# Optimization experiments

Measured on AMD Instinct MI355X. Metric: run time of the kernel, lower is better.

Reference implementation:

```python
import jax, jax.numpy as jnp
import numpy as np

N = 1 << 20          # ray samples
POS_DIM = 32         # levels * feature_dim (hash_encoding is identity stub)
DENSITY_W = 64
COLOR_W = 64


def sh4_encoding(d):
    # Fourth-order (degree-4, 16-component) real spherical harmonics, vectorized.
    x, y, z = d[..., 0], d[..., 1], d[..., 2]
    xx, yy, zz = x * x, y * y, z * z
    c0 = jnp.full_like(x, 0.28209479177387814)
    comps = [
        c0,
        0.4886025119029199 * y,
        0.4886025119029199 * z,
        0.4886025119029199 * x,
        1.0925484305920792 * x * y,
        1.0925484305920792 * y * z,
        0.9461746957575601 * zz - 0.31539156525252,
        1.0925484305920792 * x * z,
        0.5462742152960396 * (xx - yy),
        0.5900435899266435 * y * (3 * xx - yy),
        2.890611442640554 * x * y * z,
        0.4570457994644658 * y * (5 * zz - 1),
        0.3731763325901154 * z * (5 * zz - 3),
        0.4570457994644658 * x * (5 * zz - 1),
        1.445305721320277 * z * (xx - yy),
        0.5900435899266435 * x * (xx - 3 * yy),
    ]
    return jnp.stack(comps, axis=-1)  # [..., 16]


def setup_inputs() -> dict:
    key = jax.random.key(0)
    ks = jax.random.split(key, 8)
    def dense_init(k, fan_in, fan_out):
        # flax default: lecun_normal kernel, zeros bias
        w = jax.random.normal(k, (fan_in, fan_out), dtype=jnp.float32) / np.sqrt(fan_in)
        b = jnp.zeros((fan_out,), dtype=jnp.float32)
        return w, b
    position = jax.random.normal(ks[0], (N, POS_DIM), dtype=jnp.float32)
    direction = jax.random.normal(ks[1], (N, 3), dtype=jnp.float32)
    W1, b1 = dense_init(ks[2], POS_DIM, DENSITY_W)
    W2, b2 = dense_init(ks[3], DENSITY_W, 16)
    W3, b3 = dense_init(ks[4], 16 + 16, COLOR_W)
    W4, b4 = dense_init(ks[5], COLOR_W, COLOR_W)
    W5, b5 = dense_init(ks[6], COLOR_W, 3)
    return {
        "position": position, "direction": direction,
        "W1": W1, "b1": b1, "W2": W2, "b2": b2,
        "W3": W3, "b3": b3, "W4": W4, "b4": b4,
        "W5": W5, "b5": b5,
    }


def reference(position, direction, W1, b1, W2, b2, W3, b3, W4, b4, W5, b5):
    # Density MLP
    h = jax.nn.relu(position @ W1 + b1)        # [N, 64]
    density = h @ W2 + b2                      # [N, 16]
    # Color MLP on concat(density_feat, SH(dir))
    enc_dir = sh4_encoding(direction)          # [N, 16]
    c = jnp.concatenate([density, enc_dir], axis=-1)  # [N, 32]
    c = jax.nn.relu(c @ W3 + b3)               # [N, 64]
    c = jax.nn.relu(c @ W4 + b4)               # [N, 64]
    c = c @ W5 + b5                            # [N, 3]
    color = jax.nn.sigmoid(c)                  # high_dynamic_range=False
    return (density, color)
```

## Files before the change

kernel.cpp:

```cpp
#include <hip/hip_runtime.h>
#include <hip/hip_bf16.h>

typedef __bf16 bf16_t;
typedef short  s4    __attribute__((ext_vector_type(4)));
typedef short  s8    __attribute__((ext_vector_type(8)));
typedef float  f32x4 __attribute__((ext_vector_type(4)));

#define TPW   16
#define WAVES 4
#define ROWS_PER_BLOCK (WAVES * TPW * 16)

__device__ __forceinline__ short bfs(float f) {
    return __builtin_bit_cast(short, (bf16_t)f);
}
__device__ __forceinline__ s4 pack4(f32x4 a) {
    s4 r; r[0]=bfs(a[0]); r[1]=bfs(a[1]); r[2]=bfs(a[2]); r[3]=bfs(a[3]); return r;
}
__device__ __forceinline__ s4 relu_pack4(f32x4 a) {
    s4 r;
    r[0]=bfs(fmaxf(a[0],0.f)); r[1]=bfs(fmaxf(a[1],0.f));
    r[2]=bfs(fmaxf(a[2],0.f)); r[3]=bfs(fmaxf(a[3],0.f));
    return r;
}
__device__ __forceinline__ s8 cat(s4 a, s4 b) {
    return __builtin_shufflevector(a, b, 0, 1, 2, 3, 4, 5, 6, 7);
}
#define MFMA32(a,b,c) __builtin_amdgcn_mfma_f32_16x16x32_bf16(a, b, c, 0, 0, 0)

__global__ __launch_bounds__(256) void nerf_fused(
    const float* __restrict__ pos, const float* __restrict__ dir,
    const float* __restrict__ W1, const float* __restrict__ b1,
    const float* __restrict__ W2, const float* __restrict__ b2,
    const float* __restrict__ W3, const float* __restrict__ b3,
    const float* __restrict__ W4, const float* __restrict__ b4,
    const float* __restrict__ W5, const float* __restrict__ b5,
    float* __restrict__ outD, float* __restrict__ outC)
{
    const int tid  = threadIdx.x;
    const int w    = tid >> 6;
    const int lane = tid & 63;
    const int q    = lane >> 4;
    const int n    = lane & 15;

    s8 wa1[4], wa2x[2], wa3[4], wa4x[4][2], wa5x[2];
    #pragma unroll
    for (int t = 0; t < 4; ++t)
        #pragma unroll
        for (int h = 0; h < 2; ++h)
            #pragma unroll
            for (int i = 0; i < 4; ++i)
                wa1[t][4*h+i] = bfs(W1[(16*h + 4*q + i) * 64 + 16*t + n]);
    #pragma unroll
    for (int j = 0; j < 2; ++j)
        #pragma unroll
        for (int h = 0; h < 2; ++h)
            #pragma unroll
            for (int i = 0; i < 4; ++i)
                wa2x[j][4*h+i] = bfs(W2[(16*(2*j+h) + 4*q + i) * 16 + n]);
    #pragma unroll
    for (int t = 0; t < 4; ++t)
        #pragma unroll
        for (int h = 0; h < 2; ++h)
            #pragma unroll
            for (int i = 0; i < 4; ++i)
                wa3[t][4*h+i] = bfs(W3[(16*h + 4*q + i) * 64 + 16*t + n]);
    #pragma unroll
    for (int t = 0; t < 4; ++t)
        #pragma unroll
        for (int j = 0; j < 2; ++j)
            #pragma unroll
            for (int h = 0; h < 2; ++h)
                #pragma unroll
                for (int i = 0; i < 4; ++i)
                    wa4x[t][j][4*h+i] = bfs(W4[(16*(2*j+h) + 4*q + i) * 64 + 16*t + n]);
    #pragma unroll
    for (int j = 0; j < 2; ++j)
        #pragma unroll
        for (int h = 0; h < 2; ++h)
            #pragma unroll
            for (int i = 0; i < 4; ++i)
                wa5x[j][4*h+i] = (n < 3) ? bfs(W5[(16*(2*j+h) + 4*q + i) * 3 + n])
                                         : (short)0;

    f32x4 bi1[4], bi3[4], bi4[4], bi2, bi5;
    #pragma unroll
    for (int t = 0; t < 4; ++t)
        #pragma unroll
        for (int r = 0; r < 4; ++r) {
            bi1[t][r] = b1[16*t + 4*q + r];
            bi3[t][r] = b3[16*t + 4*q + r];
            bi4[t][r] = b4[16*t + 4*q + r];
        }
    #pragma unroll
    for (int r = 0; r < 4; ++r) {
        bi2[r] = b2[4*q + r];
        bi5[r] = (q == 0 && r < 3) ? b5[r] : 0.f;
    }

    const int waveRow0 = blockIdx.x * ROWS_PER_BLOCK + w * (TPW * 16);

    const float* pp = pos  + (size_t)(waveRow0 + n) * 32 + 4*q;
    const float* dp = dir  + (size_t)(waveRow0 + n) * 3;
    float*       pD = outD + (size_t)(waveRow0 + n) * 16 + 4*q;
    float*       pC = outC + (size_t)(waveRow0 + n) * 3;

    f32x4 pa = *(const f32x4*)pp;
    f32x4 pb = *(const f32x4*)(pp + 16);
    float dx = dp[0];
    float dy = dp[1];
    float dz = dp[2];

    for (int t = 0; t < TPW; ++t) {
        const float* ppn = pp + ((t + 1 < TPW) ? 16 * 32 : 0);
        const float* dpn = dp + ((t + 1 < TPW) ? 16 * 3  : 0);
        f32x4 pa2 = *(const f32x4*)ppn;
        f32x4 pb2 = *(const f32x4*)(ppn + 16);
        float dx2 = dpn[0];
        float dy2 = dpn[1];
        float dz2 = dpn[2];

        s8 xb = cat(pack4(pa), pack4(pb));

        s4 hf[4];
        #pragma unroll
        for (int tt = 0; tt < 4; ++tt) {
            f32x4 h = MFMA32(wa1[tt], xb, bi1[tt]);
            hf[tt] = relu_pack4(h);
        }

        f32x4 d2 = MFMA32(wa2x[0], cat(hf[0], hf[1]), bi2);
        d2 = MFMA32(wa2x[1], cat(hf[2], hf[3]), d2);

        *(f32x4*)pD = d2;

        f32x4 shv;
        {
            const float xx = dx*dx, yy = dy*dy, zz = dz*dz;
            if (q == 0) {
                shv[0] = 0.28209479177387814f;
                shv[1] = 0.4886025119029199f * dy;
                shv[2] = 0.4886025119029199f * dz;
                shv[3] = 0.4886025119029199f * dx;
            } else if (q == 1) {
                shv[0] = 1.0925484305920792f * dx * dy;
                shv[1] = 1.0925484305920792f * dy * dz;
                shv[2] = 0.9461746957575601f * zz - 0.31539156525252f;
                shv[3] = 1.0925484305920792f * dx * dz;
            } else if (q == 2) {
                shv[0] = 0.5462742152960396f * (xx - yy);
                shv[1] = 0.5900435899266435f * dy * (3.f*xx - yy);
                shv[2] = 2.890611442640554f * dx * dy * dz;
                shv[3] = 0.4570457994644658f * dy * (5.f*zz - 1.f);
            } else {
                shv[0] = 0.3731763325901154f * dz * (5.f*zz - 3.f);
                shv[1] = 0.4570457994644658f * dx * (5.f*zz - 1.f);
                shv[2] = 1.445305721320277f  * dz * (xx - yy);
                shv[3] = 0.5900435899266435f * dx * (xx - 3.f*yy);
            }
        }
        s8 cf = cat(pack4(d2), pack4(shv));

        s4 gf[4];
        #pragma unroll
        for (int tt = 0; tt < 4; ++tt) {
            f32x4 g = MFMA32(wa3[tt], cf, bi3[tt]);
            gf[tt] = relu_pack4(g);
        }

        s8 gl = cat(gf[0], gf[1]), gh = cat(gf[2], gf[3]);
        s4 ef[4];
        #pragma unroll
        for (int tt = 0; tt < 4; ++tt) {
            f32x4 e = MFMA32(wa4x[tt][0], gl, bi4[tt]);
            e = MFMA32(wa4x[tt][1], gh, e);
            ef[tt] = relu_pack4(e);
        }

        f32x4 c5 = MFMA32(wa5x[0], cat(ef[0], ef[1]), bi5);
        c5 = MFMA32(wa5x[1], cat(ef[2], ef[3]), c5);

        f32x4 cv;
        cv[0] = 1.f / (1.f + __expf(-c5[0]));
        cv[1] = 1.f / (1.f + __expf(-c5[1]));
        cv[2] = 1.f / (1.f + __expf(-c5[2]));
        if (q == 0) {
            pC[0] = cv[0];
            pC[1] = cv[1];
            pC[2] = cv[2];
        }

        pp += 16 * 32; dp += 16 * 3; pD += 16 * 16; pC += 16 * 3;
        pa = pa2; pb = pb2; dx = dx2; dy = dy2; dz = dz2;
    }
}

extern "C" void kernel_launch(void* const* d_in, const int* in_sizes, int n_in,
                              void* d_out, int out_size, void* d_ws, size_t ws_size,
                              hipStream_t stream) {
    const float* pos = (const float*)d_in[0];
    const float* dir = (const float*)d_in[1];
    const float* W1  = (const float*)d_in[2];
    const float* b1  = (const float*)d_in[3];
    const float* W2  = (const float*)d_in[4];
    const float* b2  = (const float*)d_in[5];
    const float* W3  = (const float*)d_in[6];
    const float* b3  = (const float*)d_in[7];
    const float* W4  = (const float*)d_in[8];
    const float* b4  = (const float*)d_in[9];
    const float* W5  = (const float*)d_in[10];
    const float* b5  = (const float*)d_in[11];

    const int N = in_sizes[0] / 32;
    float* outD = (float*)d_out;
    float* outC = outD + (size_t)N * 16;

    const int grid = N / ROWS_PER_BLOCK;
    nerf_fused<<<grid, WAVES * 64, 0, stream>>>(pos, dir, W1, b1, W2, b2, W3, b3,
                                                W4, b4, W5, b5, outD, outC);
}
```

Baseline: 253.7 us.

## Stagger per-wave tile order and raise wave priority around MFMA bursts

Each wave now starts its 16-tile loop at a different rotated tile index (4*w), so the four waves in a block touch different memory regions at the same time. MFMA groups are wrapped in s_setprio high/low so a wave that is issuing matrix ops keeps issuing ahead of waves doing loads or VALU work. The layer-4 MFMAs are also interleaved across output tiles to break the back-to-back accumulator dependency. The goal is better overlap of memory and matrix work between waves. The cost is extra address arithmetic and a wrapped prefetch index on the last iteration.

```diff
diff --git a/kernel.cpp b/kernel.cpp
--- a/kernel.cpp
+++ b/kernel.cpp
@@ -26,6 +26,8 @@
     return __builtin_shufflevector(a, b, 0, 1, 2, 3, 4, 5, 6, 7);
 }
 #define MFMA32(a,b,c) __builtin_amdgcn_mfma_f32_16x16x32_bf16(a, b, c, 0, 0, 0)
+#define PRIO_HI() __builtin_amdgcn_s_setprio(1)
+#define PRIO_LO() __builtin_amdgcn_s_setprio(0)
 
 __global__ __launch_bounds__(256) void nerf_fused(
     const float* __restrict__ pos, const float* __restrict__ dir,
@@ -99,39 +101,44 @@
 
     const int waveRow0 = blockIdx.x * ROWS_PER_BLOCK + w * (TPW * 16);
 
-    const float* pp = pos  + (size_t)(waveRow0 + n) * 32 + 4*q;
-    const float* dp = dir  + (size_t)(waveRow0 + n) * 3;
-    float*       pD = outD + (size_t)(waveRow0 + n) * 16 + 4*q;
-    float*       pC = outC + (size_t)(waveRow0 + n) * 3;
-
-    f32x4 pa = *(const f32x4*)pp;
-    f32x4 pb = *(const f32x4*)(pp + 16);
-    float dx = dp[0];
-    float dy = dp[1];
-    float dz = dp[2];
+    const float* pp0 = pos  + (size_t)(waveRow0 + n) * 32 + 4*q;
+    const float* dp0 = dir  + (size_t)(waveRow0 + n) * 3;
+    float*       pD0 = outD + (size_t)(waveRow0 + n) * 16 + 4*q;
+    float*       pC0 = outC + (size_t)(waveRow0 + n) * 3;
+
+    int r = (4 * w) & 15;
+
+    f32x4 pa = *(const f32x4*)(pp0 + r * 512);
+    f32x4 pb = *(const f32x4*)(pp0 + r * 512 + 16);
+    float dx = dp0[r * 48 + 0], dy = dp0[r * 48 + 1], dz = dp0[r * 48 + 2];
 
     for (int t = 0; t < TPW; ++t) {
-        const float* ppn = pp + ((t + 1 < TPW) ? 16 * 32 : 0);
-        const float* dpn = dp + ((t + 1 < TPW) ? 16 * 3  : 0);
-        f32x4 pa2 = *(const f32x4*)ppn;
-        f32x4 pb2 = *(const f32x4*)(ppn + 16);
-        float dx2 = dpn[0];
-        float dy2 = dpn[1];
-        float dz2 = dpn[2];
+        const int rn = (r + 1) & 15;
+        f32x4 pa2 = *(const f32x4*)(pp0 + rn * 512);
+        f32x4 pb2 = *(const f32x4*)(pp0 + rn * 512 + 16);
+        float dx2 = dp0[rn * 48 + 0], dy2 = dp0[rn * 48 + 1], dz2 = dp0[rn * 48 + 2];
 
         s8 xb = cat(pack4(pa), pack4(pb));
 
         s4 hf[4];
-        #pragma unroll
-        for (int tt = 0; tt < 4; ++tt) {
-            f32x4 h = MFMA32(wa1[tt], xb, bi1[tt]);
-            hf[tt] = relu_pack4(h);
-        }
-
+        {
+            f32x4 h0, h1, h2, h3;
+            PRIO_HI();
+            h0 = MFMA32(wa1[0], xb, bi1[0]);
+            h1 = MFMA32(wa1[1], xb, bi1[1]);
+            h2 = MFMA32(wa1[2], xb, bi1[2]);
+            h3 = MFMA32(wa1[3], xb, bi1[3]);
+            PRIO_LO();
+            hf[0] = relu_pack4(h0); hf[1] = relu_pack4(h1);
+            hf[2] = relu_pack4(h2); hf[3] = relu_pack4(h3);
+        }
+
+        PRIO_HI();
         f32x4 d2 = MFMA32(wa2x[0], cat(hf[0], hf[1]), bi2);
         d2 = MFMA32(wa2x[1], cat(hf[2], hf[3]), d2);
-
-        *(f32x4*)pD = d2;
+        PRIO_LO();
+
+        *(f32x4*)(pD0 + r * 256) = d2;
 
         f32x4 shv;
         {
@@ -161,35 +168,53 @@
         s8 cf = cat(pack4(d2), pack4(shv));
 
         s4 gf[4];
-        #pragma unroll
-        for (int tt = 0; tt < 4; ++tt) {
-            f32x4 g = MFMA32(wa3[tt], cf, bi3[tt]);
-            gf[tt] = relu_pack4(g);
+        {
+            f32x4 g0, g1, g2, g3;
+            PRIO_HI();
+            g0 = MFMA32(wa3[0], cf, bi3[0]);
+            g1 = MFMA32(wa3[1], cf, bi3[1]);
+            g2 = MFMA32(wa3[2], cf, bi3[2]);
+            g3 = MFMA32(wa3[3], cf, bi3[3]);
+            PRIO_LO();
+            gf[0] = relu_pack4(g0); gf[1] = relu_pack4(g1);
+            gf[2] = relu_pack4(g2); gf[3] = relu_pack4(g3);
         }
 
         s8 gl = cat(gf[0], gf[1]), gh = cat(gf[2], gf[3]);
         s4 ef[4];
-        #pragma unroll
-        for (int tt = 0; tt < 4; ++tt) {
-            f32x4 e = MFMA32(wa4x[tt][0], gl, bi4[tt]);
-            e = MFMA32(wa4x[tt][1], gh, e);
-            ef[tt] = relu_pack4(e);
-        }
-
+        {
+            f32x4 e0, e1, e2, e3;
+            PRIO_HI();
+            e0 = MFMA32(wa4x[0][0], gl, bi4[0]);
+            e1 = MFMA32(wa4x[1][0], gl, bi4[1]);
+            e2 = MFMA32(wa4x[2][0], gl, bi4[2]);
+            e3 = MFMA32(wa4x[3][0], gl, bi4[3]);
+            e0 = MFMA32(wa4x[0][1], gh, e0);
+            e1 = MFMA32(wa4x[1][1], gh, e1);
+            e2 = MFMA32(wa4x[2][1], gh, e2);
+            e3 = MFMA32(wa4x[3][1], gh, e3);
+            PRIO_LO();
+            ef[0] = relu_pack4(e0); ef[1] = relu_pack4(e1);
+            ef[2] = relu_pack4(e2); ef[3] = relu_pack4(e3);
+        }
+
+        PRIO_HI();
         f32x4 c5 = MFMA32(wa5x[0], cat(ef[0], ef[1]), bi5);
         c5 = MFMA32(wa5x[1], cat(ef[2], ef[3]), c5);
+        PRIO_LO();
 
         f32x4 cv;
         cv[0] = 1.f / (1.f + __expf(-c5[0]));
         cv[1] = 1.f / (1.f + __expf(-c5[1]));
         cv[2] = 1.f / (1.f + __expf(-c5[2]));
         if (q == 0) {
-            pC[0] = cv[0];
-            pC[1] = cv[1];
-            pC[2] = cv[2];
-        }
-
-        pp += 16 * 32; dp += 16 * 3; pD += 16 * 16; pC += 16 * 3;
+            float* pc = pC0 + r * 48;
+            pc[0] = cv[0];
+            pc[1] = cv[1];
+            pc[2] = cv[2];
+        }
+
+        r = rn;
         pa = pa2; pb = pb2; dx = dx2; dy = dy2; dz = dz2;
     }
 }
```

After: 266.6 us. +5.1%, slower.
